# Kernel optimization log

Measured on AMD Instinct MI355X. Metric: run time of the kernel, lower is better.

The kernel has to match this reference:

```python
import jax, jax.numpy as jnp
import numpy as np

N_POIS = 100000
N_HYPEREDGES = 50000
NNZ = 1600000
D = 256
NUM_LAYERS = 2
P_DROP = 0.3


def setup_inputs() -> dict:
    key = jax.random.key(0)
    ks = jax.random.split(key, 10)
    scale = 1.0 / (1.0 - P_DROP)
    drop1 = jax.random.bernoulli(ks[4], 1.0 - P_DROP, (NUM_LAYERS, N_POIS, D)).astype(jnp.float32) * scale
    drop2 = jax.random.bernoulli(ks[5], 1.0 - P_DROP, (NUM_LAYERS, N_POIS, D)).astype(jnp.float32) * scale
    return {
        "pois_embs": jax.random.normal(ks[0], (N_POIS, D), dtype=jnp.float32),
        "tar_vals": jax.random.uniform(ks[1], (NNZ,), dtype=jnp.float32),
        "src_vals": jax.random.uniform(ks[2], (NNZ,), dtype=jnp.float32),
        "layer_attention": jnp.ones((NUM_LAYERS + 1,), dtype=jnp.float32),
        "drop1": drop1,
        "drop2": drop2,
        "tar_rows": jax.random.randint(ks[6], (NNZ,), 0, N_HYPEREDGES, dtype=jnp.int32),
        "tar_cols": jax.random.randint(ks[7], (NNZ,), 0, N_POIS, dtype=jnp.int32),
        "src_rows": jax.random.randint(ks[8], (NNZ,), 0, N_POIS, dtype=jnp.int32),
        "src_cols": jax.random.randint(ks[9], (NNZ,), 0, N_HYPEREDGES, dtype=jnp.int32),
    }


def _spmm(rows, cols, vals, dense, num_rows):
    # COO sparse @ dense: gather rows of `dense` by cols, scale, scatter-add by rows
    return jax.ops.segment_sum(vals[:, None] * dense[cols], rows, num_segments=num_rows)


def reference(pois_embs, tar_vals, src_vals, layer_attention, drop1, drop2,
              tar_rows, tar_cols, src_rows, src_cols):
    embs = pois_embs
    layer_outs = [embs]
    for i in range(NUM_LAYERS):
        # msg_tar = HG_poi_tar @ embs  -> [n_hyperedges, d]
        msg_tar = _spmm(tar_rows, tar_cols, tar_vals, embs, N_HYPEREDGES)
        # msg_src = HG_poi_src @ msg_tar -> [n_pois, d]
        msg_src = _spmm(src_rows, src_cols, src_vals, msg_tar, N_POIS)
        msg_src = jax.nn.relu(msg_src) * drop1[i]      # conv-layer dropout
        embs = (msg_src + layer_outs[-1]) * drop2[i]   # residual + F.dropout
        layer_outs.append(embs)
    w = jax.nn.softmax(layer_attention)                # [num_layers+1]
    stacked = jnp.stack(layer_outs)                    # [L+1, n_pois, d]
    return jnp.sum(stacked * w[:, None, None], axis=0)
```

## Files before the change

### kernel.cpp

```cpp
#include <hip/hip_runtime.h>

#define NPOIS 100000
#define NHYP  50000
#define NNZE  1600000
#define DIM   256

#define SH_TAR 6
#define SH_SRC 7
#define NBUCK 782
#define CHUNK 6250

typedef unsigned int uint;

#define DROP_C ((float)(1.0 / (1.0 - 0.3)))

__device__ __forceinline__ uint pack_bf16(float a, float b) {
    uint ua = __float_as_uint(a); ua += 0x7fffu + ((ua >> 16) & 1u);
    uint ub = __float_as_uint(b); ub += 0x7fffu + ((ub >> 16) & 1u);
    return (ua >> 16) | (ub & 0xffff0000u);
}
__device__ __forceinline__ float4 unpack_h(uint2 u) {
    return make_float4(__uint_as_float(u.x << 16), __uint_as_float(u.x & 0xffff0000u),
                       __uint_as_float(u.y << 16), __uint_as_float(u.y & 0xffff0000u));
}

__global__ __launch_bounds__(256) void to_h_kernel(
    const float4* __restrict__ in, uint2* __restrict__ out, int n4)
{
    int stride = gridDim.x * blockDim.x;
    for (int i = blockIdx.x * blockDim.x + threadIdx.x; i < n4; i += stride) {
        float4 x = in[i];
        out[i] = make_uint2(pack_bf16(x.x, x.y), pack_bf16(x.z, x.w));
    }
}

__global__ __launch_bounds__(256) void drop_bits_kernel(
    const float4* __restrict__ d1, const float4* __restrict__ d2,
    uint* __restrict__ o1, uint* __restrict__ o2, int nw)
{
    int t = blockIdx.x * blockDim.x + threadIdx.x;
    if (t >= 2 * nw) return;
    const float4* src = (t < nw) ? d1 : d2;
    uint* dst = (t < nw) ? o1 : o2;
    int w = (t < nw) ? t : t - nw;
    uint m = 0;
#pragma unroll
    for (int q = 0; q < 8; ++q) {
        float4 v = src[(size_t)w * 8 + q];
        m |= (v.x != 0.f ? 1u : 0u) << (4 * q);
        m |= (v.y != 0.f ? 2u : 0u) << (4 * q);
        m |= (v.z != 0.f ? 4u : 0u) << (4 * q);
        m |= (v.w != 0.f ? 8u : 0u) << (4 * q);
    }
    dst[w] = m;
}


__global__ __launch_bounds__(256) void hist_coarse(
    const int* __restrict__ tr, const int* __restrict__ sr,
    int* __restrict__ c_tar, int* __restrict__ c_src, int nnz)
{
    __shared__ int lt[NBUCK], ls[NBUCK];
    int t = threadIdx.x;
    int s = blockIdx.x * CHUNK, e = min(s + CHUNK, nnz);
    for (int i = t; i < NBUCK; i += 256) { lt[i] = 0; ls[i] = 0; }
    __syncthreads();
    for (int i = s + t; i < e; i += 256) {
        atomicAdd(&lt[tr[i] >> SH_TAR], 1);
        atomicAdd(&ls[sr[i] >> SH_SRC], 1);
    }
    __syncthreads();
    for (int i = t; i < NBUCK; i += 256) {
        if (lt[i]) atomicAdd(&c_tar[i], lt[i]);
        if (ls[i]) atomicAdd(&c_src[i], ls[i]);
    }
}

__global__ __launch_bounds__(256) void scan_offsets(
    const int* __restrict__ c_tar, const int* __restrict__ c_src,
    int* __restrict__ off_tar, int* __restrict__ tl_tar,
    int* __restrict__ off_src, int* __restrict__ tl_src)
{
    __shared__ int lds[256];
    int t = threadIdx.x;
    for (int sel = 0; sel < 2; ++sel) {
        const int* c = sel ? c_src : c_tar;
        int* off = sel ? off_src : off_tar;
        int* tl  = sel ? tl_src : tl_tar;
        int carry = 0;
        for (int base = 0; base < NBUCK; base += 256) {
            int i = base + t;
            int v = (i < NBUCK) ? c[i] : 0;
            lds[t] = v;
            __syncthreads();
            for (int o = 1; o < 256; o <<= 1) {
                int x = (t >= o) ? lds[t - o] : 0;
                __syncthreads();
                lds[t] += x;
                __syncthreads();
            }
            int excl = carry + lds[t] - v;
            if (i < NBUCK) { off[i] = excl; tl[i] = excl; }
            carry += lds[255];
            __syncthreads();
        }
        if (t == 0) off[NBUCK] = carry;
        __syncthreads();
    }
}

__global__ __launch_bounds__(256) void csr_stage(
    const int* __restrict__ tar_rows, const int* __restrict__ tar_cols,
    const float* __restrict__ tar_vals,
    const int* __restrict__ src_rows, const int* __restrict__ src_cols,
    const float* __restrict__ src_vals,
    int* __restrict__ tl_tar, uint2* __restrict__ stag_tar,
    int* __restrict__ tl_src, uint2* __restrict__ stag_src, int nnz)
{
    __shared__ int lh[NBUCK];
    __shared__ int lbase[NBUCK];
    int t = threadIdx.x;
    bool is_src = blockIdx.x >= 256;
    int blk = is_src ? blockIdx.x - 256 : blockIdx.x;
    const int* rows = is_src ? src_rows : tar_rows;
    const int* cols = is_src ? src_cols : tar_cols;
    const float* vals = is_src ? src_vals : tar_vals;
    int* tails = is_src ? tl_src : tl_tar;
    uint2* stag = is_src ? stag_src : stag_tar;
    const int SH = is_src ? SH_SRC : SH_TAR;

    int s = blk * CHUNK, e = min(s + CHUNK, nnz);
    for (int i = t; i < NBUCK; i += 256) lh[i] = 0;
    __syncthreads();
    for (int i = s + t; i < e; i += 256) atomicAdd(&lh[rows[i] >> SH], 1);
    __syncthreads();
    for (int i = t; i < NBUCK; i += 256) {
        int c = lh[i];
        lbase[i] = c ? atomicAdd(&tails[i], c) : 0;
        lh[i] = 0;
    }
    __syncthreads();
    for (int i = s + t; i < e; i += 256) {
        int r = rows[i];
        int b = r >> SH;
        int pos = lbase[b] + atomicAdd(&lh[b], 1);
        uint uv = __float_as_uint(vals[i]);
        uv += 0x7fffu + ((uv >> 16) & 1u);
        stag[pos] = make_uint2((uint)r, ((uint)cols[i] << 15) | ((uv >> 16) & 0x7fffu));
    }
}

__global__ __launch_bounds__(256) void csr_finalize(
    const uint2* __restrict__ stag_tar, const int* __restrict__ off_tar,
    int* __restrict__ rp_tar, uint* __restrict__ ep_tar,
    const uint2* __restrict__ stag_src, const int* __restrict__ off_src,
    int* __restrict__ rp_src, uint* __restrict__ ep_src, int nnz)
{
    __shared__ uint2 recs[4096];
    __shared__ int lhist[128];
    __shared__ int lbase[129];
    bool is_src = blockIdx.x >= NBUCK;
    int b = is_src ? blockIdx.x - NBUCK : blockIdx.x;
    const uint2* stag = is_src ? stag_src : stag_tar;
    const int* off = is_src ? off_src : off_tar;
    int* rp = is_src ? rp_src : rp_tar;
    uint* ep = is_src ? ep_src : ep_tar;
    const int SH = is_src ? SH_SRC : SH_TAR;
    const int RPB = 1 << SH;
    const int nrows = is_src ? NPOIS : NHYP;
    int t = threadIdx.x;
    int base = off[b];
    int n = off[b + 1] - base;
    int r0 = b << SH;

    for (int i = t; i < RPB; i += 256) lhist[i] = 0;
    __syncthreads();

    bool fit = (n <= 4096);
    for (int i = t; i < n; i += 256) {
        uint2 rec = stag[base + i];
        if (fit) recs[i] = rec;
        atomicAdd(&lhist[(int)rec.x - r0], 1);
    }
    __syncthreads();
    if (t == 0) {
        int run = 0;
        for (int i = 0; i < RPB; ++i) { lbase[i] = run; run += lhist[i]; }
        lbase[RPB] = run;
    }
    __syncthreads();
    for (int i = t; i < RPB; i += 256) {
        int rg = r0 + i;
        if (rg < nrows) rp[rg] = base + lbase[i];
    }
    if (b == 0 && t == 0) rp[nrows] = nnz;
    for (int i = t; i < RPB; i += 256) lhist[i] = 0;
    __syncthreads();
    for (int i = t; i < n; i += 256) {
        uint2 rec = fit ? recs[i] : stag[base + i];
        int rl = (int)rec.x - r0;
        int slot = lbase[rl] + atomicAdd(&lhist[rl], 1);
        ep[base + slot] = rec.y;
    }
}

#define GCH 8

__device__ __forceinline__ float4 gather_h(
    const int* __restrict__ rp, const uint* __restrict__ ep,
    const uint2* __restrict__ dh, int row, int lane)
{
    int s = rp[row], e = rp[row + 1];
    float4 acc = {0.f, 0.f, 0.f, 0.f};
    for (int k = s; k < e; k += GCH) {
        uint ev[GCH];
#pragma unroll
        for (int j = 0; j < GCH; ++j)
            ev[j] = (k + j < e) ? ep[k + j] : 0u;
        uint2 x[GCH];
#pragma unroll
        for (int j = 0; j < GCH; ++j)
            x[j] = dh[(size_t)(ev[j] >> 15) * (DIM / 4) + lane];
#pragma unroll
        for (int j = 0; j < GCH; ++j) {
            float vv = __uint_as_float((ev[j] & 0x7fffu) << 16);
            acc.x += vv * __uint_as_float(x[j].x << 16);
            acc.y += vv * __uint_as_float(x[j].x & 0xffff0000u);
            acc.z += vv * __uint_as_float(x[j].y << 16);
            acc.w += vv * __uint_as_float(x[j].y & 0xffff0000u);
        }
    }
    return acc;
}

__device__ __forceinline__ float4 gather_f(
    const int* __restrict__ rp, const uint* __restrict__ ep,
    const float4* __restrict__ d4, int row, int lane)
{
    int s = rp[row], e = rp[row + 1];
    float4 acc = {0.f, 0.f, 0.f, 0.f};
    for (int k = s; k < e; k += GCH) {
        uint ev[GCH];
#pragma unroll
        for (int j = 0; j < GCH; ++j)
            ev[j] = (k + j < e) ? ep[k + j] : 0u;
        float4 x[GCH];
#pragma unroll
        for (int j = 0; j < GCH; ++j)
            x[j] = d4[(size_t)(ev[j] >> 15) * (DIM / 4) + lane];
#pragma unroll
        for (int j = 0; j < GCH; ++j) {
            float vv = __uint_as_float((ev[j] & 0x7fffu) << 16);
            acc.x += vv * x[j].x;
            acc.y += vv * x[j].y;
            acc.z += vv * x[j].z;
            acc.w += vv * x[j].w;
        }
    }
    return acc;
}

__device__ __forceinline__ float4 drop4(const uint* __restrict__ bm, int row, int lane)
{
    uint m = bm[(size_t)row * 8 + (lane >> 3)] >> ((lane & 7) * 4);
    return make_float4((m & 1u) ? DROP_C : 0.f, (m & 2u) ? DROP_C : 0.f,
                       (m & 4u) ? DROP_C : 0.f, (m & 8u) ? DROP_C : 0.f);
}

template <bool BF16D>
__global__ __launch_bounds__(256) void spmm_to_h(
    const int* __restrict__ rp, const uint* __restrict__ ep,
    const void* __restrict__ dense, uint2* __restrict__ out_h, int nrows)
{
    int wid  = (blockIdx.x * blockDim.x + threadIdx.x) >> 6;
    int lane = threadIdx.x & 63;
    if (wid >= nrows) return;
    int row = __builtin_amdgcn_readfirstlane(wid);
    float4 a = BF16D ? gather_h(rp, ep, (const uint2*)dense, row, lane)
                     : gather_f(rp, ep, (const float4*)dense, row, lane);
    out_h[(size_t)row * (DIM / 4) + lane] = make_uint2(pack_bf16(a.x, a.y), pack_bf16(a.z, a.w));
}

template <bool PH, bool BITS>
__global__ __launch_bounds__(256) void spmm_epi1(
    const int* __restrict__ rp, const uint* __restrict__ ep,
    const uint2* __restrict__ msg_h,
    const uint2* __restrict__ pois_h, const float4* __restrict__ pois_f,
    const float4* __restrict__ d1, const float4* __restrict__ d2,
    const uint* __restrict__ bm1, const uint* __restrict__ bm2,
    uint2* __restrict__ out_h, int nrows)
{
    int wid  = (blockIdx.x * blockDim.x + threadIdx.x) >> 6;
    int lane = threadIdx.x & 63;
    if (wid >= nrows) return;
    int row = __builtin_amdgcn_readfirstlane(wid);
    size_t idx = (size_t)row * (DIM / 4) + lane;
    float4 a, b;
    if (BITS) { a = drop4(bm1, row, lane); b = drop4(bm2, row, lane); }
    else      { a = d1[idx]; b = d2[idx]; }
    float4 p = PH ? unpack_h(pois_h[idx]) : pois_f[idx];
    float4 m = gather_h(rp, ep, msg_h, row, lane);
    float4 r;
    r.x = (fmaxf(m.x, 0.f) * a.x + p.x) * b.x;
    r.y = (fmaxf(m.y, 0.f) * a.y + p.y) * b.y;
    r.z = (fmaxf(m.z, 0.f) * a.z + p.z) * b.z;
    r.w = (fmaxf(m.w, 0.f) * a.w + p.w) * b.w;
    out_h[idx] = make_uint2(pack_bf16(r.x, r.y), pack_bf16(r.z, r.w));
}

template <bool PH, bool BITS>
__global__ __launch_bounds__(256) void spmm_final(
    const int* __restrict__ rp, const uint* __restrict__ ep,
    const uint2* __restrict__ msg_h,
    const uint2* __restrict__ pois_h, const float4* __restrict__ pois_f,
    const uint2* __restrict__ embs1_h,
    const float4* __restrict__ d1, const float4* __restrict__ d2,
    const uint* __restrict__ bm1, const uint* __restrict__ bm2,
    const float* __restrict__ attn, float4* __restrict__ out, int nrows)
{
    int wid  = (blockIdx.x * blockDim.x + threadIdx.x) >> 6;
    int lane = threadIdx.x & 63;
    if (wid >= nrows) return;
    int row = __builtin_amdgcn_readfirstlane(wid);

    float a0 = attn[0], a1 = attn[1], a2 = attn[2];
    float mx = fmaxf(a0, fmaxf(a1, a2));
    float e0 = __expf(a0 - mx), e1 = __expf(a1 - mx), e2 = __expf(a2 - mx);
    float inv = 1.f / (e0 + e1 + e2);
    float w0 = e0 * inv, w1 = e1 * inv, w2 = e2 * inv;

    size_t idx = (size_t)row * (DIM / 4) + lane;
    float4 a, b;
    if (BITS) { a = drop4(bm1, row, lane); b = drop4(bm2, row, lane); }
    else      { a = d1[idx]; b = d2[idx]; }
    float4 p0 = PH ? unpack_h(pois_h[idx]) : pois_f[idx];
    float4 p1 = unpack_h(embs1_h[idx]);
    float4 m = gather_h(rp, ep, msg_h, row, lane);
    float4 r;
    r.x = w0 * p0.x + w1 * p1.x + w2 * ((fmaxf(m.x, 0.f) * a.x + p1.x) * b.x);
    r.y = w0 * p0.y + w1 * p1.y + w2 * ((fmaxf(m.y, 0.f) * a.y + p1.y) * b.y);
    r.z = w0 * p0.z + w1 * p1.z + w2 * ((fmaxf(m.z, 0.f) * a.z + p1.z) * b.z);
    r.w = w0 * p0.w + w1 * p1.w + w2 * ((fmaxf(m.w, 0.f) * a.w + p1.w) * b.w);
    out[idx] = r;
}

extern "C" void kernel_launch(void* const* d_in, const int* in_sizes, int n_in,
                              void* d_out, int out_size, void* d_ws, size_t ws_size,
                              hipStream_t stream)
{
    const float* pois     = (const float*)d_in[0];
    const float* tar_vals = (const float*)d_in[1];
    const float* src_vals = (const float*)d_in[2];
    const float* attn     = (const float*)d_in[3];
    const float* drop1    = (const float*)d_in[4];
    const float* drop2    = (const float*)d_in[5];
    const int*   tar_rows = (const int*)d_in[6];
    const int*   tar_cols = (const int*)d_in[7];
    const int*   src_rows = (const int*)d_in[8];
    const int*   src_cols = (const int*)d_in[9];
    float* out = (float*)d_out;

    const size_t ptn = (size_t)NPOIS * DIM;

    char* p = (char*)d_ws;
    uint* ep_tar   = (uint*)p;              p += (size_t)NNZE * 4;
    uint* ep_src   = (uint*)p;              p += (size_t)NNZE * 4;
    int*  rp_tar   = (int*)p;               p += 200064;
    int*  rp_src   = (int*)p;               p += 400064;
    int*  misc     = (int*)p;               p += 32768;
    uint2* msg_h   = (uint2*)p;             p += (size_t)NHYP * DIM * 2;
    uint2* embs1_h = (uint2*)p;             p += (size_t)NPOIS * DIM * 2;

    const size_t bits_words = (size_t)2 * NPOIS * 8;
    uint* bits1 = (uint*)p;
    uint* bits2 = bits1 + bits_words;       p += 2 * bits_words * 4;
    size_t bits_need = (size_t)(p - (char*)d_ws);
    bool have_bits = ws_size >= bits_need;

    uint2* pois_h  = (uint2*)p;
    bool full = ws_size >= bits_need + ptn * 2;

    int* cntc_tar = misc;
    int* off_tar  = cntc_tar + NBUCK;
    int* tl_tar   = off_tar + NBUCK + 1;
    int* cntc_src = tl_tar + NBUCK;
    int* off_src  = cntc_src + NBUCK;
    int* tl_src   = off_src + NBUCK + 1;

    uint2* stag_tar = (uint2*)msg_h;
    uint2* stag_src = stag_tar + NNZE;

    const int BLK = 256;

    if (full)
        to_h_kernel<<<(int)(ptn / 4 + BLK - 1) / BLK, BLK, 0, stream>>>(
            (const float4*)pois, pois_h, (int)(ptn / 4));

    if (have_bits) {
        int nw = (int)(2 * ptn / 32);
        drop_bits_kernel<<<(2 * nw + BLK - 1) / BLK, BLK, 0, stream>>>(
            (const float4*)drop1, (const float4*)drop2, bits1, bits2, nw);
    }

    hipMemsetAsync(misc, 0, 32768, stream);
    hist_coarse<<<256, BLK, 0, stream>>>(tar_rows, src_rows, cntc_tar, cntc_src, NNZE);
    scan_offsets<<<1, BLK, 0, stream>>>(cntc_tar, cntc_src, off_tar, tl_tar, off_src, tl_src);
    csr_stage<<<512, BLK, 0, stream>>>(
        tar_rows, tar_cols, tar_vals, src_rows, src_cols, src_vals,
        tl_tar, stag_tar, tl_src, stag_src, NNZE);
    csr_finalize<<<2 * NBUCK, BLK, 0, stream>>>(
        stag_tar, off_tar, rp_tar, ep_tar,
        stag_src, off_src, rp_src, ep_src, NNZE);

    const int gb_hyp = NHYP / 4;
    const int gb_poi = NPOIS / 4;

    const float4* d1_l0 = (const float4*)drop1;
    const float4* d2_l0 = (const float4*)drop2;
    const float4* d1_l1 = (const float4*)(drop1 + ptn);
    const float4* d2_l1 = (const float4*)(drop2 + ptn);
    const uint* b1_l0 = bits1;
    const uint* b2_l0 = bits2;
    const uint* b1_l1 = bits1 + (size_t)NPOIS * 8;
    const uint* b2_l1 = bits2 + (size_t)NPOIS * 8;

    if (full)
        spmm_to_h<true><<<gb_hyp, BLK, 0, stream>>>(rp_tar, ep_tar, pois_h, msg_h, NHYP);
    else
        spmm_to_h<false><<<gb_hyp, BLK, 0, stream>>>(rp_tar, ep_tar, pois, msg_h, NHYP);

    if (full && have_bits)
        spmm_epi1<true, true><<<gb_poi, BLK, 0, stream>>>(
            rp_src, ep_src, msg_h, pois_h, (const float4*)pois,
            d1_l0, d2_l0, b1_l0, b2_l0, embs1_h, NPOIS);
    else if (full)
        spmm_epi1<true, false><<<gb_poi, BLK, 0, stream>>>(
            rp_src, ep_src, msg_h, pois_h, (const float4*)pois,
            d1_l0, d2_l0, b1_l0, b2_l0, embs1_h, NPOIS);
    else if (have_bits)
        spmm_epi1<false, true><<<gb_poi, BLK, 0, stream>>>(
            rp_src, ep_src, msg_h, pois_h, (const float4*)pois,
            d1_l0, d2_l0, b1_l0, b2_l0, embs1_h, NPOIS);
    else
        spmm_epi1<false, false><<<gb_poi, BLK, 0, stream>>>(
            rp_src, ep_src, msg_h, pois_h, (const float4*)pois,
            d1_l0, d2_l0, b1_l0, b2_l0, embs1_h, NPOIS);

    spmm_to_h<true><<<gb_hyp, BLK, 0, stream>>>(rp_tar, ep_tar, embs1_h, msg_h, NHYP);

    if (full && have_bits)
        spmm_final<true, true><<<gb_poi, BLK, 0, stream>>>(
            rp_src, ep_src, msg_h, pois_h, (const float4*)pois, embs1_h,
            d1_l1, d2_l1, b1_l1, b2_l1, attn, (float4*)out, NPOIS);
    else if (full)
        spmm_final<true, false><<<gb_poi, BLK, 0, stream>>>(
            rp_src, ep_src, msg_h, pois_h, (const float4*)pois, embs1_h,
            d1_l1, d2_l1, b1_l1, b2_l1, attn, (float4*)out, NPOIS);
    else if (have_bits)
        spmm_final<false, true><<<gb_poi, BLK, 0, stream>>>(
            rp_src, ep_src, msg_h, pois_h, (const float4*)pois, embs1_h,
            d1_l1, d2_l1, b1_l1, b2_l1, attn, (float4*)out, NPOIS);
    else
        spmm_final<false, false><<<gb_poi, BLK, 0, stream>>>(
            rp_src, ep_src, msg_h, pois_h, (const float4*)pois, embs1_h,
            d1_l1, d2_l1, b1_l1, b2_l1, attn, (float4*)out, NPOIS);
}
```

Measured before the change: 1.184 ms.

## Quantize hyperedge messages to int8 with per-row scale and fuse prep kernels

The intermediate hyperedge message matrix is now stored as int8 with one float scale per row instead of bf16. This halves the bytes fetched by the random row gathers in the second SpMM of each layer. Separately, the bf16 conversion, dropout-bitmask packing and coarse histogram kernels are merged into one launch to cut launch overhead. The risk is a loss of precision, since the max-abs int8 quantization may exceed the tolerance, plus an extra scale load on every gathered row.

Result: faster. 1.059 ms (-10.6%).

```diff
diff --git a/kernel.cpp b/kernel.cpp
--- a/kernel.cpp
+++ b/kernel.cpp
@@ -14,6 +14,20 @@
 
 #define DROP_C ((float)(1.0 / (1.0 - 0.3)))
 
+#define OFF_EPT   0
+#define OFF_EPS   6400000
+#define OFF_RPT   12800000
+#define OFF_RPS   13000064
+#define OFF_MISC  13400128
+#define OFF_MSG   13432896
+#define OFF_SC    26232896
+#define OFF_EMB   39032896
+#define OFF_BITS1 90232896
+#define OFF_BITS2 96632896
+#define OFF_POISH 103032896
+#define NEED_BITS 103032896
+#define NEED_FULL 154232896
+
 __device__ __forceinline__ uint pack_bf16(float a, float b) {
     uint ua = __float_as_uint(a); ua += 0x7fffu + ((ua >> 16) & 1u);
     uint ub = __float_as_uint(b); ub += 0x7fffu + ((ub >> 16) & 1u);
@@ -24,55 +38,153 @@
                        __uint_as_float(u.y << 16), __uint_as_float(u.y & 0xffff0000u));
 }
 
-__global__ __launch_bounds__(256) void to_h_kernel(
-    const float4* __restrict__ in, uint2* __restrict__ out, int n4)
-{
-    int stride = gridDim.x * blockDim.x;
-    for (int i = blockIdx.x * blockDim.x + threadIdx.x; i < n4; i += stride) {
-        float4 x = in[i];
-        out[i] = make_uint2(pack_bf16(x.x, x.y), pack_bf16(x.z, x.w));
-    }
-}
-
-__global__ __launch_bounds__(256) void drop_bits_kernel(
+#define GCH 8
+
+__device__ __forceinline__ float4 gather_h(
+    const int* __restrict__ rp, const uint* __restrict__ ep,
+    const uint2* __restrict__ dh, int row, int lane)
+{
+    int s = rp[row], e = rp[row + 1];
+    float4 acc = {0.f, 0.f, 0.f, 0.f};
+    for (int k = s; k < e; k += GCH) {
+        uint ev[GCH];
+#pragma unroll
+        for (int j = 0; j < GCH; ++j)
+            ev[j] = (k + j < e) ? ep[k + j] : 0u;
+        uint2 x[GCH];
+#pragma unroll
+        for (int j = 0; j < GCH; ++j)
+            x[j] = dh[(size_t)(ev[j] >> 15) * (DIM / 4) + lane];
+#pragma unroll
+        for (int j = 0; j < GCH; ++j) {
+            float vv = __uint_as_float((ev[j] & 0x7fffu) << 16);
+            acc.x += vv * __uint_as_float(x[j].x << 16);
+            acc.y += vv * __uint_as_float(x[j].x & 0xffff0000u);
+            acc.z += vv * __uint_as_float(x[j].y << 16);
+            acc.w += vv * __uint_as_float(x[j].y & 0xffff0000u);
+        }
+    }
+    return acc;
+}
+
+__device__ __forceinline__ float4 gather_f(
+    const int* __restrict__ rp, const uint* __restrict__ ep,
+    const float4* __restrict__ d4, int row, int lane)
+{
+    int s = rp[row], e = rp[row + 1];
+    float4 acc = {0.f, 0.f, 0.f, 0.f};
+    for (int k = s; k < e; k += GCH) {
+        uint ev[GCH];
+#pragma unroll
+        for (int j = 0; j < GCH; ++j)
+            ev[j] = (k + j < e) ? ep[k + j] : 0u;
+        float4 x[GCH];
+#pragma unroll
+        for (int j = 0; j < GCH; ++j)
+            x[j] = d4[(size_t)(ev[j] >> 15) * (DIM / 4) + lane];
+#pragma unroll
+        for (int j = 0; j < GCH; ++j) {
+            float vv = __uint_as_float((ev[j] & 0x7fffu) << 16);
+            acc.x += vv * x[j].x;
+            acc.y += vv * x[j].y;
+            acc.z += vv * x[j].z;
+            acc.w += vv * x[j].w;
+        }
+    }
+    return acc;
+}
+
+__device__ __forceinline__ float4 gather_q(
+    const int* __restrict__ rp, const uint* __restrict__ ep,
+    const uint* __restrict__ mq, const float* __restrict__ sc,
+    int row, int lane)
+{
+    int s = rp[row], e = rp[row + 1];
+    float4 acc = {0.f, 0.f, 0.f, 0.f};
+    for (int k = s; k < e; k += GCH) {
+        uint ev[GCH];
+#pragma unroll
+        for (int j = 0; j < GCH; ++j)
+            ev[j] = (k + j < e) ? ep[k + j] : 0u;
+        uint x[GCH]; float st[GCH];
+#pragma unroll
+        for (int j = 0; j < GCH; ++j) {
+            uint c = ev[j] >> 15;
+            x[j]  = mq[(size_t)c * 64 + lane];
+            st[j] = sc[c];
+        }
+#pragma unroll
+        for (int j = 0; j < GCH; ++j) {
+            float vv = __uint_as_float((ev[j] & 0x7fffu) << 16) * st[j];
+            acc.x += vv * (float)((int)(x[j] << 24) >> 24);
+            acc.y += vv * (float)((int)(x[j] << 16) >> 24);
+            acc.z += vv * (float)((int)(x[j] <<  8) >> 24);
+            acc.w += vv * (float)((int)x[j] >> 24);
+        }
+    }
+    return acc;
+}
+
+__device__ __forceinline__ float4 drop4(const uint* __restrict__ bm, int row, int lane)
+{
+    uint m = bm[(size_t)row * 8 + (lane >> 3)] >> ((lane & 7) * 4);
+    return make_float4((m & 1u) ? DROP_C : 0.f, (m & 2u) ? DROP_C : 0.f,
+                       (m & 4u) ? DROP_C : 0.f, (m & 8u) ? DROP_C : 0.f);
+}
+
+__global__ __launch_bounds__(256) void prep_kernel(
+    const float4* __restrict__ pois, uint2* __restrict__ pois_h,
     const float4* __restrict__ d1, const float4* __restrict__ d2,
-    uint* __restrict__ o1, uint* __restrict__ o2, int nw)
-{
-    int t = blockIdx.x * blockDim.x + threadIdx.x;
-    if (t >= 2 * nw) return;
-    const float4* src = (t < nw) ? d1 : d2;
-    uint* dst = (t < nw) ? o1 : o2;
-    int w = (t < nw) ? t : t - nw;
-    uint m = 0;
-#pragma unroll
-    for (int q = 0; q < 8; ++q) {
-        float4 v = src[(size_t)w * 8 + q];
-        m |= (v.x != 0.f ? 1u : 0u) << (4 * q);
-        m |= (v.y != 0.f ? 2u : 0u) << (4 * q);
-        m |= (v.z != 0.f ? 4u : 0u) << (4 * q);
-        m |= (v.w != 0.f ? 8u : 0u) << (4 * q);
-    }
-    dst[w] = m;
-}
-
-
-__global__ __launch_bounds__(256) void hist_coarse(
+    uint* __restrict__ o1, uint* __restrict__ o2,
     const int* __restrict__ tr, const int* __restrict__ sr,
-    int* __restrict__ c_tar, int* __restrict__ c_src, int nnz)
+    int* __restrict__ c_tar, int* __restrict__ c_src,
+    int full, int have_bits)
 {
     __shared__ int lt[NBUCK], ls[NBUCK];
-    int t = threadIdx.x;
-    int s = blockIdx.x * CHUNK, e = min(s + CHUNK, nnz);
-    for (int i = t; i < NBUCK; i += 256) { lt[i] = 0; ls[i] = 0; }
-    __syncthreads();
-    for (int i = s + t; i < e; i += 256) {
-        atomicAdd(&lt[tr[i] >> SH_TAR], 1);
-        atomicAdd(&ls[sr[i] >> SH_SRC], 1);
-    }
-    __syncthreads();
-    for (int i = t; i < NBUCK; i += 256) {
-        if (lt[i]) atomicAdd(&c_tar[i], lt[i]);
-        if (ls[i]) atomicAdd(&c_src[i], ls[i]);
+    int b = blockIdx.x, t = threadIdx.x;
+    if (b < 256) {
+        int s = b * CHUNK, e = s + CHUNK;
+        for (int i = t; i < NBUCK; i += 256) { lt[i] = 0; ls[i] = 0; }
+        __syncthreads();
+        for (int i = s + t; i < e; i += 256) {
+            atomicAdd(&lt[tr[i] >> SH_TAR], 1);
+            atomicAdd(&ls[sr[i] >> SH_SRC], 1);
+        }
+        __syncthreads();
+        for (int i = t; i < NBUCK; i += 256) {
+            if (lt[i]) atomicAdd(&c_tar[i], lt[i]);
+            if (ls[i]) atomicAdd(&c_src[i], ls[i]);
+        }
+        return;
+    }
+    int base_bits = 256;
+    if (have_bits && b < base_bits + 12500) {
+        const int nw = 1600000;
+        int w = (b - base_bits) * 256 + t;
+        if (w < 2 * nw) {
+            const float4* src = (w < nw) ? d1 : d2;
+            uint* dst = (w < nw) ? o1 : o2;
+            int ww = (w < nw) ? w : w - nw;
+            uint m = 0;
+#pragma unroll
+            for (int q = 0; q < 8; ++q) {
+                float4 v = src[(size_t)ww * 8 + q];
+                m |= (v.x != 0.f ? 1u : 0u) << (4 * q);
+                m |= (v.y != 0.f ? 2u : 0u) << (4 * q);
+                m |= (v.z != 0.f ? 4u : 0u) << (4 * q);
+                m |= (v.w != 0.f ? 8u : 0u) << (4 * q);
+            }
+            dst[ww] = m;
+        }
+        return;
+    }
+    if (full) {
+        int base_toh = 256 + (have_bits ? 12500 : 0);
+        int i = (b - base_toh) * 256 + t;
+        if (i < NPOIS * (DIM / 4)) {
+            float4 x = pois[i];
+            pois_h[i] = make_uint2(pack_bf16(x.x, x.y), pack_bf16(x.z, x.w));
+        }
     }
 }
 
@@ -175,7 +287,6 @@
 
     for (int i = t; i < RPB; i += 256) lhist[i] = 0;
     __syncthreads();
-
     bool fit = (n <= 4096);
     for (int i = t; i < n; i += 256) {
         uint2 rec = stag[base + i];
@@ -204,73 +315,11 @@
     }
 }
 
-#define GCH 8
-
-__device__ __forceinline__ float4 gather_h(
-    const int* __restrict__ rp, const uint* __restrict__ ep,
-    const uint2* __restrict__ dh, int row, int lane)
-{
-    int s = rp[row], e = rp[row + 1];
-    float4 acc = {0.f, 0.f, 0.f, 0.f};
-    for (int k = s; k < e; k += GCH) {
-        uint ev[GCH];
-#pragma unroll
-        for (int j = 0; j < GCH; ++j)
-            ev[j] = (k + j < e) ? ep[k + j] : 0u;
-        uint2 x[GCH];
-#pragma unroll
-        for (int j = 0; j < GCH; ++j)
-            x[j] = dh[(size_t)(ev[j] >> 15) * (DIM / 4) + lane];
-#pragma unroll
-        for (int j = 0; j < GCH; ++j) {
-            float vv = __uint_as_float((ev[j] & 0x7fffu) << 16);
-            acc.x += vv * __uint_as_float(x[j].x << 16);
-            acc.y += vv * __uint_as_float(x[j].x & 0xffff0000u);
-            acc.z += vv * __uint_as_float(x[j].y << 16);
-            acc.w += vv * __uint_as_float(x[j].y & 0xffff0000u);
-        }
-    }
-    return acc;
-}
-
-__device__ __forceinline__ float4 gather_f(
-    const int* __restrict__ rp, const uint* __restrict__ ep,
-    const float4* __restrict__ d4, int row, int lane)
-{
-    int s = rp[row], e = rp[row + 1];
-    float4 acc = {0.f, 0.f, 0.f, 0.f};
-    for (int k = s; k < e; k += GCH) {
-        uint ev[GCH];
-#pragma unroll
-        for (int j = 0; j < GCH; ++j)
-            ev[j] = (k + j < e) ? ep[k + j] : 0u;
-        float4 x[GCH];
-#pragma unroll
-        for (int j = 0; j < GCH; ++j)
-            x[j] = d4[(size_t)(ev[j] >> 15) * (DIM / 4) + lane];
-#pragma unroll
-        for (int j = 0; j < GCH; ++j) {
-            float vv = __uint_as_float((ev[j] & 0x7fffu) << 16);
-            acc.x += vv * x[j].x;
-            acc.y += vv * x[j].y;
-            acc.z += vv * x[j].z;
-            acc.w += vv * x[j].w;
-        }
-    }
-    return acc;
-}
-
-__device__ __forceinline__ float4 drop4(const uint* __restrict__ bm, int row, int lane)
-{
-    uint m = bm[(size_t)row * 8 + (lane >> 3)] >> ((lane & 7) * 4);
-    return make_float4((m & 1u) ? DROP_C : 0.f, (m & 2u) ? DROP_C : 0.f,
-                       (m & 4u) ? DROP_C : 0.f, (m & 8u) ? DROP_C : 0.f);
-}
-
 template <bool BF16D>
 __global__ __launch_bounds__(256) void spmm_to_h(
     const int* __restrict__ rp, const uint* __restrict__ ep,
-    const void* __restrict__ dense, uint2* __restrict__ out_h, int nrows)
+    const void* __restrict__ dense, uint* __restrict__ mq,
+    float* __restrict__ sc, int nrows)
 {
     int wid  = (blockIdx.x * blockDim.x + threadIdx.x) >> 6;
     int lane = threadIdx.x & 63;
@@ -278,13 +327,24 @@
     int row = __builtin_amdgcn_readfirstlane(wid);
     float4 a = BF16D ? gather_h(rp, ep, (const uint2*)dense, row, lane)
                      : gather_f(rp, ep, (const float4*)dense, row, lane);
-    out_h[(size_t)row * (DIM / 4) + lane] = make_uint2(pack_bf16(a.x, a.y), pack_bf16(a.z, a.w));
+    float am = fmaxf(fmaxf(fabsf(a.x), fabsf(a.y)), fmaxf(fabsf(a.z), fabsf(a.w)));
+#pragma unroll
+    for (int m = 1; m < 64; m <<= 1) am = fmaxf(am, __shfl_xor(am, m, 64));
+    float inv = am > 0.f ? 127.f / am : 0.f;
+    int q0 = __float2int_rn(a.x * inv);
+    int q1 = __float2int_rn(a.y * inv);
+    int q2 = __float2int_rn(a.z * inv);
+    int q3 = __float2int_rn(a.w * inv);
+    mq[(size_t)row * 64 + lane] =
+        (uint)(q0 & 0xff) | ((uint)(q1 & 0xff) << 8) |
+        ((uint)(q2 & 0xff) << 16) | ((uint)q3 << 24);
+    if (lane == 0) sc[row] = am * (1.f / 127.f);
 }
 
 template <bool PH, bool BITS>
 __global__ __launch_bounds__(256) void spmm_epi1(
     const int* __restrict__ rp, const uint* __restrict__ ep,
-    const uint2* __restrict__ msg_h,
+    const uint* __restrict__ mq, const float* __restrict__ sc,
     const uint2* __restrict__ pois_h, const float4* __restrict__ pois_f,
     const float4* __restrict__ d1, const float4* __restrict__ d2,
     const uint* __restrict__ bm1, const uint* __restrict__ bm2,
@@ -299,7 +359,7 @@
     if (BITS) { a = drop4(bm1, row, lane); b = drop4(bm2, row, lane); }
     else      { a = d1[idx]; b = d2[idx]; }
     float4 p = PH ? unpack_h(pois_h[idx]) : pois_f[idx];
-    float4 m = gather_h(rp, ep, msg_h, row, lane);
+    float4 m = gather_q(rp, ep, mq, sc, row, lane);
     float4 r;
     r.x = (fmaxf(m.x, 0.f) * a.x + p.x) * b.x;
     r.y = (fmaxf(m.y, 0.f) * a.y + p.y) * b.y;
@@ -311,7 +371,7 @@
 template <bool PH, bool BITS>
 __global__ __launch_bounds__(256) void spmm_final(
     const int* __restrict__ rp, const uint* __restrict__ ep,
-    const uint2* __restrict__ msg_h,
+    const uint* __restrict__ mq, const float* __restrict__ sc,
     const uint2* __restrict__ pois_h, const float4* __restrict__ pois_f,
     const uint2* __restrict__ embs1_h,
     const float4* __restrict__ d1, const float4* __restrict__ d2,
@@ -335,7 +395,7 @@
     else      { a = d1[idx]; b = d2[idx]; }
     float4 p0 = PH ? unpack_h(pois_h[idx]) : pois_f[idx];
     float4 p1 = unpack_h(embs1_h[idx]);
-    float4 m = gather_h(rp, ep, msg_h, row, lane);
+    float4 m = gather_q(rp, ep, mq, sc, row, lane);
     float4 r;
     r.x = w0 * p0.x + w1 * p1.x + w2 * ((fmaxf(m.x, 0.f) * a.x + p1.x) * b.x);
     r.y = w0 * p0.y + w1 * p1.y + w2 * ((fmaxf(m.y, 0.f) * a.y + p1.y) * b.y);
@@ -358,27 +418,24 @@
     const int*   tar_cols = (const int*)d_in[7];
     const int*   src_rows = (const int*)d_in[8];
     const int*   src_cols = (const int*)d_in[9];
-    float* out = (float*)d_out;
+    float4* out = (float4*)d_out;
+    char* ws = (char*)d_ws;
 
     const size_t ptn = (size_t)NPOIS * DIM;
-
-    char* p = (char*)d_ws;
-    uint* ep_tar   = (uint*)p;              p += (size_t)NNZE * 4;
-    uint* ep_src   = (uint*)p;              p += (size_t)NNZE * 4;
-    int*  rp_tar   = (int*)p;               p += 200064;
-    int*  rp_src   = (int*)p;               p += 400064;
-    int*  misc     = (int*)p;               p += 32768;
-    uint2* msg_h   = (uint2*)p;             p += (size_t)NHYP * DIM * 2;
-    uint2* embs1_h = (uint2*)p;             p += (size_t)NPOIS * DIM * 2;
-
-    const size_t bits_words = (size_t)2 * NPOIS * 8;
-    uint* bits1 = (uint*)p;
-    uint* bits2 = bits1 + bits_words;       p += 2 * bits_words * 4;
-    size_t bits_need = (size_t)(p - (char*)d_ws);
-    bool have_bits = ws_size >= bits_need;
-
-    uint2* pois_h  = (uint2*)p;
-    bool full = ws_size >= bits_need + ptn * 2;
+    int have_bits = ws_size >= (size_t)NEED_BITS ? 1 : 0;
+    int full      = ws_size >= (size_t)NEED_FULL ? 1 : 0;
+
+    uint*  ep_tar  = (uint*)(ws + OFF_EPT);
+    uint*  ep_src  = (uint*)(ws + OFF_EPS);
+    int*   rp_tar  = (int*)(ws + OFF_RPT);
+    int*   rp_src  = (int*)(ws + OFF_RPS);
+    int*   misc    = (int*)(ws + OFF_MISC);
+    uint*  msg_q   = (uint*)(ws + OFF_MSG);
+    float* msg_sc  = (float*)(ws + OFF_SC);
+    uint2* embs1_h = (uint2*)(ws + OFF_EMB);
+    uint*  bits1   = (uint*)(ws + OFF_BITS1);
+    uint*  bits2   = (uint*)(ws + OFF_BITS2);
+    uint2* pois_h  = (uint2*)(ws + OFF_POISH);
 
     int* cntc_tar = misc;
     int* off_tar  = cntc_tar + NBUCK;
@@ -387,23 +444,18 @@
     int* off_src  = cntc_src + NBUCK;
     int* tl_src   = off_src + NBUCK + 1;
 
-    uint2* stag_tar = (uint2*)msg_h;
+    uint2* stag_tar = (uint2*)(ws + OFF_MSG);
     uint2* stag_src = stag_tar + NNZE;
 
     const int BLK = 256;
 
-    if (full)
-        to_h_kernel<<<(int)(ptn / 4 + BLK - 1) / BLK, BLK, 0, stream>>>(
-            (const float4*)pois, pois_h, (int)(ptn / 4));
-
-    if (have_bits) {
-        int nw = (int)(2 * ptn / 32);
-        drop_bits_kernel<<<(2 * nw + BLK - 1) / BLK, BLK, 0, stream>>>(
-            (const float4*)drop1, (const float4*)drop2, bits1, bits2, nw);
-    }
-
     hipMemsetAsync(misc, 0, 32768, stream);
-    hist_coarse<<<256, BLK, 0, stream>>>(tar_rows, src_rows, cntc_tar, cntc_src, NNZE);
+    int prep_grid = 256 + (have_bits ? 12500 : 0) + (full ? 25000 : 0);
+    prep_kernel<<<prep_grid, BLK, 0, stream>>>(
+        (const float4*)pois, pois_h,
+        (const float4*)drop1, (const float4*)drop2, bits1, bits2,
+        tar_rows, src_rows, cntc_tar, cntc_src, full, have_bits);
+
     scan_offsets<<<1, BLK, 0, stream>>>(cntc_tar, cntc_src, off_tar, tl_tar, off_src, tl_src);
     csr_stage<<<512, BLK, 0, stream>>>(
         tar_rows, tar_cols, tar_vals, src_rows, src_cols, src_vals,
@@ -425,43 +477,43 @@
     const uint* b2_l1 = bits2 + (size_t)NPOIS * 8;
 
     if (full)
-        spmm_to_h<true><<<gb_hyp, BLK, 0, stream>>>(rp_tar, ep_tar, pois_h, msg_h, NHYP);
+        spmm_to_h<true><<<gb_hyp, BLK, 0, stream>>>(rp_tar, ep_tar, pois_h, msg_q, msg_sc, NHYP);
     else
-        spmm_to_h<false><<<gb_hyp, BLK, 0, stream>>>(rp_tar, ep_tar, pois, msg_h, NHYP);
+        spmm_to_h<false><<<gb_hyp, BLK, 0, stream>>>(rp_tar, ep_tar, pois, msg_q, msg_sc, NHYP);
 
     if (full && have_bits)
         spmm_epi1<true, true><<<gb_poi, BLK, 0, stream>>>(
-            rp_src, ep_src, msg_h, pois_h, (const float4*)pois,
+            rp_src, ep_src, msg_q, msg_sc, pois_h, (const float4*)pois,
             d1_l0, d2_l0, b1_l0, b2_l0, embs1_h, NPOIS);
     else if (full)
         spmm_epi1<true, false><<<gb_poi, BLK, 0, stream>>>(
-            rp_src, ep_src, msg_h, pois_h, (const float4*)pois,
+            rp_src, ep_src, msg_q, msg_sc, pois_h, (const float4*)pois,
             d1_l0, d2_l0, b1_l0, b2_l0, embs1_h, NPOIS);
     else if (have_bits)
         spmm_epi1<false, true><<<gb_poi, BLK, 0, stream>>>(
-            rp_src, ep_src, msg_h, pois_h, (const float4*)pois,
+            rp_src, ep_src, msg_q, msg_sc, pois_h, (const float4*)pois,
             d1_l0, d2_l0, b1_l0, b2_l0, embs1_h, NPOIS);
     else
         spmm_epi1<false, false><<<gb_poi, BLK, 0, stream>>>(
-            rp_src, ep_src, msg_h, pois_h, (const float4*)pois,
+            rp_src, ep_src, msg_q, msg_sc, pois_h, (const float4*)pois,
             d1_l0, d2_l0, b1_l0, b2_l0, embs1_h, NPOIS);
 
-    spmm_to_h<true><<<gb_hyp, BLK, 0, stream>>>(rp_tar, ep_tar, embs1_h, msg_h, NHYP);
+    spmm_to_h<true><<<gb_hyp, BLK, 0, stream>>>(rp_tar, ep_tar, embs1_h, msg_q, msg_sc, NHYP);
 
     if (full && have_bits)
         spmm_final<true, true><<<gb_poi, BLK, 0, stream>>>(
-            rp_src, ep_src, msg_h, pois_h, (const float4*)pois, embs1_h,
-            d1_l1, d2_l1, b1_l1, b2_l1, attn, (float4*)out, NPOIS);
+            rp_src, ep_src, msg_q, msg_sc, pois_h, (const float4*)pois, embs1_h,
+            d1_l1, d2_l1, b1_l1, b2_l1, attn, out, NPOIS);
     else if (full)
         spmm_final<true, false><<<gb_poi, BLK, 0, stream>>>(
-            rp_src, ep_src, msg_h, pois_h, (const float4*)pois, embs1_h,
-            d1_l1, d2_l1, b1_l1, b2_l1, attn, (float4*)out, NPOIS);
+            rp_src, ep_src, msg_q, msg_sc, pois_h, (const float4*)pois, embs1_h,
+            d1_l1, d2_l1, b1_l1, b2_l1, attn, out, NPOIS);
     else if (have_bits)
         spmm_final<false, true><<<gb_poi, BLK, 0, stream>>>(
-            rp_src, ep_src, msg_h, pois_h, (const float4*)pois, embs1_h,
-            d1_l1, d2_l1, b1_l1, b2_l1, attn, (float4*)out, NPOIS);
+            rp_src, ep_src, msg_q, msg_sc, pois_h, (const float4*)pois, embs1_h,
+            d1_l1, d2_l1, b1_l1, b2_l1, attn, out, NPOIS);
     else
         spmm_final<false, false><<<gb_poi, BLK, 0, stream>>>(
-            rp_src, ep_src, msg_h, pois_h, (const float4*)pois, embs1_h,
-            d1_l1, d2_l1, b1_l1, b2_l1, attn, (float4*)out, NPOIS);
-}
+            rp_src, ep_src, msg_q, msg_sc, pois_h, (const float4*)pois, embs1_h,
+            d1_l1, d2_l1, b1_l1, b2_l1, attn, out, NPOIS);
+}
```
